# Optimization experiments

Measured on AMD Instinct MI355X. Metric: run time of the kernel, lower is better.

Reference implementation:

```python
import jax, jax.numpy as jnp
import numpy as np

N_NODES = 50000
N_EDGES = 800000


def _glorot(key, shape):
    fan_in, fan_out = shape
    lim = float(np.sqrt(6.0 / (fan_in + fan_out)))
    return jax.random.uniform(key, shape, jnp.float32, -lim, lim)


def setup_inputs() -> dict:
    key = jax.random.key(0)
    ks = jax.random.split(key, 8)
    x = jax.random.normal(ks[0], (N_NODES, 2), jnp.float32)
    edge_index = jax.random.randint(ks[1], (2, N_EDGES), 0, N_NODES, jnp.int64)
    edge_weight = jax.random.uniform(ks[2], (N_EDGES,), jnp.float32)
    return {
        "x": x,
        "edge_index": edge_index,
        "edge_weight": edge_weight,
        "W1": _glorot(ks[3], (2, 128)),
        "b1": jnp.zeros((128,), jnp.float32),
        "W2": _glorot(ks[4], (128, 64)),
        "b2": jnp.zeros((64,), jnp.float32),
        "W3": _glorot(ks[5], (64, 1)),
        "b3": jnp.zeros((1,), jnp.float32),
    }


def _gcn_conv(x, W, b, src, dst, ew, n_nodes):
    # PyG GCNConv with normalize=False: out[i] = sum_{e:(j->i)} ew[e] * (x_j @ W) + b
    h = x @ W                       # [N, F_out] tiny GEMM
    msg = h[src] * ew[:, None]      # [E, F_out] gather + scale
    out = jax.ops.segment_sum(msg, dst, num_segments=n_nodes)  # scatter-add
    return out + b


def reference(x, edge_index, edge_weight, W1, b1, W2, b2, W3, b3):
    src, dst = edge_index[0], edge_index[1]  # source_to_target flow: aggregate at dst
    n = x.shape[0]
    h1 = jax.nn.relu(_gcn_conv(x, W1, b1, src, dst, edge_weight, n))
    # dropout is a no-op in eval mode
    h2 = jax.nn.relu(_gcn_conv(h1, W2, b2, src, dst, edge_weight, n))
    h3 = _gcn_conv(h2, W3, b3, src, dst, edge_weight, n)  # [N, 1]
    return h3.squeeze(-1)  # [N]
```

## Files before the change

kernel.cpp:

```cpp
#include <hip/hip_runtime.h>
#include <hip/hip_fp16.h>

#define N_NODES 50000
#define N_EDGES 800000
#define BSHIFT 7
#define NBKT 391
#define CAP 3072
#define TILE 2048
#define BIN_THREADS 512
#define SL_THREADS 512

typedef _Float16 f16x8 __attribute__((ext_vector_type(8)));
typedef float f32x4 __attribute__((ext_vector_type(4)));
typedef float f32x2 __attribute__((ext_vector_type(2)));

__device__ __forceinline__ float edge_w(unsigned p) {
    return __half2float(__ushort_as_half((unsigned short)(p >> 16)));
}

__device__ __forceinline__ unsigned char f32_to_fp8(float v) {
    int w = __builtin_amdgcn_cvt_pk_fp8_f32(v, v, 0, false);
    return (unsigned char)(w & 0xFF);
}

__global__ __launch_bounds__(BIN_THREADS) void bin_edges(
    const int* __restrict__ src, const int* __restrict__ dstA,
    const float* __restrict__ ew, int* __restrict__ bcur,
    uint2* __restrict__ brec) {
    __shared__ unsigned pk[TILE];
    __shared__ unsigned short sdst[TILE];
    __shared__ uint2 rec[TILE];
    __shared__ int cnt[NBKT];
    __shared__ int lofs[NBKT];
    __shared__ int cbase[NBKT];
    __shared__ int scn[BIN_THREADS];

    int t = threadIdx.x;
    int e0 = blockIdx.x * TILE;
    int nmax = N_EDGES - e0;
    if (nmax > TILE) nmax = TILE;
    if (nmax < 0) nmax = 0;
    if (t < NBKT) cnt[t] = 0;
    __syncthreads();
    for (int i = t; i < nmax; i += BIN_THREADS) {
        int e = e0 + i;
        int d = dstA[e];
        unsigned hw = (unsigned)__half_as_ushort(__float2half(ew[e]));
        pk[i] = (unsigned)src[e] | (hw << 16);
        sdst[i] = (unsigned short)d;
        atomicAdd(&cnt[d >> BSHIFT], 1);
    }
    __syncthreads();
    int v = (t < NBKT) ? cnt[t] : 0;
    scn[t] = v;
    __syncthreads();
    for (int off = 1; off < BIN_THREADS; off <<= 1) {
        int u = (t >= off) ? scn[t - off] : 0;
        __syncthreads();
        scn[t] += u;
        __syncthreads();
    }
    if (t < NBKT) {
        lofs[t] = scn[t] - v;
        cbase[t] = t * CAP + (v ? atomicAdd(&bcur[t], v) : 0);
        cnt[t] = 0;
    }
    __syncthreads();
    for (int i = t; i < nmax; i += BIN_THREADS) {
        int d = sdst[i];
        int bk = d >> BSHIFT;
        int pos = lofs[bk] + atomicAdd(&cnt[bk], 1);
        rec[pos] = make_uint2(pk[i], (unsigned)d);
    }
    __syncthreads();
    for (int i = t; i < nmax; i += BIN_THREADS) {
        uint2 r = rec[i];
        int bk = (int)(r.y >> BSHIFT);
        int g = cbase[bk] + (i - lofs[bk]);
        brec[g] = r;
    }
}

__global__ __launch_bounds__(SL_THREADS) void sort_l1(
    const int* __restrict__ bcur, const uint2* __restrict__ brec,
    const float* __restrict__ x,
    const float* __restrict__ W1, const float* __restrict__ b1,
    const float* __restrict__ W2,
    unsigned* __restrict__ sorted, int2* __restrict__ rowspan,
    unsigned char* __restrict__ t2) {
    __shared__ unsigned spk[CAP];
    __shared__ unsigned short sdl[CAP];
    __shared__ int nh[128], scn[128], lcur[128];
    __shared__ float nodeA[128], nodeB[128];
    __shared__ __align__(16) __half w2t[64][136];
    __shared__ __align__(16) float w1r0[128];
    __shared__ __align__(16) float w1r1[128];
    __shared__ __align__(16) float b1s[128];

    int b = blockIdx.x;
    int t = threadIdx.x;
    int base = b * CAP;
    int n = bcur[b];
    if (n > CAP) n = CAP;

    for (int idx = t; idx < 128 * 64; idx += SL_THREADS) {
        int k = idx >> 6, nn = idx & 63;
        w2t[nn][k] = __float2half(W2[idx]);
    }
    if (t < 128) {
        w1r0[t] = W1[t];
        w1r1[t] = W1[128 + t];
        b1s[t]  = b1[t];
        nh[t] = 0;
        lcur[t] = 0;
        nodeA[t] = 0.f;
        nodeB[t] = 0.f;
    }
    __syncthreads();

    for (int e = t; e < n; e += SL_THREADS) {
        uint2 r = brec[base + e];
        spk[e] = r.x;
        int d = (int)(r.y & 127u);
        sdl[e] = (unsigned short)d;
        atomicAdd(&nh[d], 1);
    }
    __syncthreads();

    int vv = 0;
    if (t < 128) { vv = nh[t]; scn[t] = vv; }
    __syncthreads();
    for (int off = 1; off < 128; off <<= 1) {
        int u = (t < 128 && t >= off) ? scn[t - off] : 0;
        __syncthreads();
        if (t < 128) scn[t] += u;
        __syncthreads();
    }
    if (t < 128) {
        int ex = scn[t] - vv;
        int node = (b << BSHIFT) + t;
        if (node < N_NODES) rowspan[node] = make_int2(base + ex, base + ex + vv);
        nh[t] = ex;
    }
    __syncthreads();

    for (int e = t; e < n; e += SL_THREADS) {
        unsigned p = spk[e];
        int dlow = sdl[e];
        int pos = base + nh[dlow] + atomicAdd(&lcur[dlow], 1);
        sorted[pos] = p;
        float w = edge_w(p);
        float2 xv = ((const float2*)x)[p & 0xFFFF];
        atomicAdd(&nodeA[dlow], w * xv.x);
        atomicAdd(&nodeB[dlow], w * xv.y);
    }
    __syncthreads();

    int wave = t >> 6, lane = t & 63;
    int m0 = wave * 16;
    int fr = lane & 15;
    int kb = (lane >> 4) * 8;
    float a0 = nodeA[m0 + fr];
    float a1 = nodeB[m0 + fr];
    f32x4 acc0 = {0.f, 0.f, 0.f, 0.f};
    f32x4 acc1 = {0.f, 0.f, 0.f, 0.f};
    f32x4 acc2 = {0.f, 0.f, 0.f, 0.f};
    f32x4 acc3 = {0.f, 0.f, 0.f, 0.f};
#pragma unroll
    for (int k0 = 0; k0 < 128; k0 += 32) {
        f16x8 av;
#pragma unroll
        for (int j = 0; j < 8; j++) {
            int k = k0 + kb + j;
            float h = fmaxf(fmaf(a0, w1r0[k], fmaf(a1, w1r1[k], b1s[k])), 0.f);
            av[j] = (_Float16)h;
        }
        f16x8 bv0 = *(const f16x8*)&w2t[ 0 + fr][k0 + kb];
        f16x8 bv1 = *(const f16x8*)&w2t[16 + fr][k0 + kb];
        f16x8 bv2 = *(const f16x8*)&w2t[32 + fr][k0 + kb];
        f16x8 bv3 = *(const f16x8*)&w2t[48 + fr][k0 + kb];
        acc0 = __builtin_amdgcn_mfma_f32_16x16x32_f16(av, bv0, acc0, 0, 0, 0);
        acc1 = __builtin_amdgcn_mfma_f32_16x16x32_f16(av, bv1, acc1, 0, 0, 0);
        acc2 = __builtin_amdgcn_mfma_f32_16x16x32_f16(av, bv2, acc2, 0, 0, 0);
        acc3 = __builtin_amdgcn_mfma_f32_16x16x32_f16(av, bv3, acc3, 0, 0, 0);
    }
    int rowb = (b << BSHIFT) + m0 + (lane >> 4) * 4;
#pragma unroll
    for (int r = 0; r < 4; r++) {
        int node = rowb + r;
        if (node < N_NODES) {
            unsigned char* o = t2 + node * 64 + fr;
            o[0]  = f32_to_fp8(acc0[r]);
            o[16] = f32_to_fp8(acc1[r]);
            o[32] = f32_to_fp8(acc2[r]);
            o[48] = f32_to_fp8(acc3[r]);
        }
    }
}

__global__ void gather2_dot3(const int2* __restrict__ rowspan, const unsigned* __restrict__ sorted,
                             const unsigned char* __restrict__ t2, const float* __restrict__ b2,
                             const float* __restrict__ W3, float* __restrict__ t3) {
    int gtid = blockIdx.x * blockDim.x + threadIdx.x;
    int node = gtid >> 6;
    int lane = threadIdx.x & 63;
    if (node >= N_NODES) return;
    int eg  = lane >> 3;
    int fli = lane & 7;
    int2 sp = rowspan[node];
    float a0 = 0.f, a1 = 0.f, a2 = 0.f, a3 = 0.f, a4 = 0.f, a5 = 0.f, a6 = 0.f, a7 = 0.f;
    int e = sp.x + eg;
    for (; e + 8 < sp.y; e += 16) {
        unsigned p0 = sorted[e];
        unsigned p1 = sorted[e + 8];
        uint2 q0 = *(const uint2*)(t2 + (p0 & 0xFFFF) * 64 + fli * 8);
        uint2 q1 = *(const uint2*)(t2 + (p1 & 0xFFFF) * 64 + fli * 8);
        float w0 = edge_w(p0), w1 = edge_w(p1);
        f32x2 f;
        f = __builtin_amdgcn_cvt_pk_f32_fp8(q0.x, false); a0 = fmaf(w0, f.x, a0); a1 = fmaf(w0, f.y, a1);
        f = __builtin_amdgcn_cvt_pk_f32_fp8(q0.x, true);  a2 = fmaf(w0, f.x, a2); a3 = fmaf(w0, f.y, a3);
        f = __builtin_amdgcn_cvt_pk_f32_fp8(q0.y, false); a4 = fmaf(w0, f.x, a4); a5 = fmaf(w0, f.y, a5);
        f = __builtin_amdgcn_cvt_pk_f32_fp8(q0.y, true);  a6 = fmaf(w0, f.x, a6); a7 = fmaf(w0, f.y, a7);
        f = __builtin_amdgcn_cvt_pk_f32_fp8(q1.x, false); a0 = fmaf(w1, f.x, a0); a1 = fmaf(w1, f.y, a1);
        f = __builtin_amdgcn_cvt_pk_f32_fp8(q1.x, true);  a2 = fmaf(w1, f.x, a2); a3 = fmaf(w1, f.y, a3);
        f = __builtin_amdgcn_cvt_pk_f32_fp8(q1.y, false); a4 = fmaf(w1, f.x, a4); a5 = fmaf(w1, f.y, a5);
        f = __builtin_amdgcn_cvt_pk_f32_fp8(q1.y, true);  a6 = fmaf(w1, f.x, a6); a7 = fmaf(w1, f.y, a7);
    }
    if (e < sp.y) {
        unsigned p = sorted[e];
        uint2 q = *(const uint2*)(t2 + (p & 0xFFFF) * 64 + fli * 8);
        float w = edge_w(p);
        f32x2 f;
        f = __builtin_amdgcn_cvt_pk_f32_fp8(q.x, false); a0 = fmaf(w, f.x, a0); a1 = fmaf(w, f.y, a1);
        f = __builtin_amdgcn_cvt_pk_f32_fp8(q.x, true);  a2 = fmaf(w, f.x, a2); a3 = fmaf(w, f.y, a3);
        f = __builtin_amdgcn_cvt_pk_f32_fp8(q.y, false); a4 = fmaf(w, f.x, a4); a5 = fmaf(w, f.y, a5);
        f = __builtin_amdgcn_cvt_pk_f32_fp8(q.y, true);  a6 = fmaf(w, f.x, a6); a7 = fmaf(w, f.y, a7);
    }
#pragma unroll
    for (int off = 8; off < 64; off <<= 1) {
        a0 += __shfl_xor(a0, off); a1 += __shfl_xor(a1, off);
        a2 += __shfl_xor(a2, off); a3 += __shfl_xor(a3, off);
        a4 += __shfl_xor(a4, off); a5 += __shfl_xor(a5, off);
        a6 += __shfl_xor(a6, off); a7 += __shfl_xor(a7, off);
    }
    float4 bA = *(const float4*)(b2 + fli * 8);
    float4 bB = *(const float4*)(b2 + fli * 8 + 4);
    float4 wA = *(const float4*)(W3 + fli * 8);
    float4 wB = *(const float4*)(W3 + fli * 8 + 4);
    float h = fmaxf(a0 + bA.x, 0.f) * wA.x + fmaxf(a1 + bA.y, 0.f) * wA.y +
              fmaxf(a2 + bA.z, 0.f) * wA.z + fmaxf(a3 + bA.w, 0.f) * wA.w +
              fmaxf(a4 + bB.x, 0.f) * wB.x + fmaxf(a5 + bB.y, 0.f) * wB.y +
              fmaxf(a6 + bB.z, 0.f) * wB.z + fmaxf(a7 + bB.w, 0.f) * wB.w;
#pragma unroll
    for (int off = 1; off < 8; off <<= 1) h += __shfl_xor(h, off);
    if (lane == 0) t3[node] = h;
}

__global__ void gather3(const int2* __restrict__ rowspan, const unsigned* __restrict__ sorted,
                        const float* __restrict__ t3, const float* __restrict__ b3,
                        float* __restrict__ out) {
    int gtid = blockIdx.x * blockDim.x + threadIdx.x;
    int wid = gtid >> 6;
    int lane = threadIdx.x & 63;
    int sub = lane >> 4;
    int sl  = lane & 15;
    int node = wid * 4 + sub;
    if (node >= N_NODES) return;
    int2 sp = rowspan[node];
    float acc = 0.f;
    for (int e = sp.x + sl; e < sp.y; e += 16) {
        unsigned p = sorted[e];
        acc = fmaf(edge_w(p), t3[p & 0xFFFF], acc);
    }
#pragma unroll
    for (int off = 1; off < 16; off <<= 1) acc += __shfl_xor(acc, off);
    if (sl == 0) out[node] = acc + b3[0];
}

extern "C" void kernel_launch(void* const* d_in, const int* in_sizes, int n_in,
                              void* d_out, int out_size, void* d_ws, size_t ws_size,
                              hipStream_t stream) {
    const float* x  = (const float*)d_in[0];
    const int*   ei = (const int*)d_in[1];
    const float* ew = (const float*)d_in[2];
    const float* W1 = (const float*)d_in[3];
    const float* b1 = (const float*)d_in[4];
    const float* W2 = (const float*)d_in[5];
    const float* b2 = (const float*)d_in[6];
    const float* W3 = (const float*)d_in[7];
    const float* b3 = (const float*)d_in[8];
    float* out = (float*)d_out;

    const int* src = ei;
    const int* dst = ei + N_EDGES;

    char* p = (char*)d_ws;
    int*  bcur    = (int*)p;            p += NBKT * sizeof(int);
    p = (char*)(((uintptr_t)p + 15) & ~(uintptr_t)15);
    int2* rowspan = (int2*)p;           p += N_NODES * sizeof(int2);
    uint2* brec   = (uint2*)p;          p += (long)NBKT * CAP * sizeof(uint2);
    unsigned* sorted = (unsigned*)p;    p += (long)NBKT * CAP * sizeof(unsigned);
    unsigned char* t2 = (unsigned char*)p; p += 64L * N_NODES;
    float* t3     = (float*)p;          p += N_NODES * sizeof(float);

    hipMemsetAsync(bcur, 0, NBKT * sizeof(int), stream);

    bin_edges<<<NBKT, BIN_THREADS, 0, stream>>>(src, dst, ew, bcur, brec);

    sort_l1<<<NBKT, SL_THREADS, 0, stream>>>(bcur, brec, x, W1, b1, W2, sorted, rowspan, t2);

    gather2_dot3<<<(N_NODES * 64 + 255) / 256, 256, 0, stream>>>(rowspan, sorted, t2, b2, W3, t3);

    gather3<<<((N_NODES + 3) / 4 * 64 + 255) / 256, 256, 0, stream>>>(rowspan, sorted, t3, b3, out);
}
```

Before: 139.5 us.

## Use wave-shuffle scans, register-held edges, and narrower gather3 node groups

Replaces the barrier-heavy shared-memory prefix scans in bin_edges and sort_l1 with wavefront shuffle scans plus a small cross-wave combine. In sort_l1 the records are kept in registers (up to 6 per thread), layer-1 aggregation moves into the first pass, and edges are scattered into LDS and then written to global memory contiguously instead of through scattered global writes. gather3 now assigns 8 lanes per node instead of 16, so each wave covers 8 nodes. The fixed 6-per-thread register array relies on CAP/SL_THREADS = 6, and the LDS atomic ordering still makes the within-node edge order nondeterministic.

```diff
diff --git a/kernel.cpp b/kernel.cpp
--- a/kernel.cpp
+++ b/kernel.cpp
@@ -33,9 +33,11 @@
     __shared__ int cnt[NBKT];
     __shared__ int lofs[NBKT];
     __shared__ int cbase[NBKT];
-    __shared__ int scn[BIN_THREADS];
+    __shared__ int wsum[8];
+    __shared__ int wpre[8];
 
     int t = threadIdx.x;
+    int lane = t & 63, wid = t >> 6;
     int e0 = blockIdx.x * TILE;
     int nmax = N_EDGES - e0;
     if (nmax > TILE) nmax = TILE;
@@ -52,16 +54,23 @@
     }
     __syncthreads();
     int v = (t < NBKT) ? cnt[t] : 0;
-    scn[t] = v;
-    __syncthreads();
-    for (int off = 1; off < BIN_THREADS; off <<= 1) {
-        int u = (t >= off) ? scn[t - off] : 0;
-        __syncthreads();
-        scn[t] += u;
-        __syncthreads();
-    }
+    int s = v;
+#pragma unroll
+    for (int off = 1; off < 64; off <<= 1) {
+        int u = __shfl_up(s, off);
+        if (lane >= off) s += u;
+    }
+    if (lane == 63) wsum[wid] = s;
+    __syncthreads();
+    if (t < 8) {
+        int a = 0;
+        for (int i = 0; i < t; i++) a += wsum[i];
+        wpre[t] = a;
+    }
+    __syncthreads();
+    int incl = s + wpre[wid];
     if (t < NBKT) {
-        lofs[t] = scn[t] - v;
+        lofs[t] = incl - v;
         cbase[t] = t * CAP + (v ? atomicAdd(&bcur[t], v) : 0);
         cnt[t] = 0;
     }
@@ -89,16 +98,17 @@
     unsigned* __restrict__ sorted, int2* __restrict__ rowspan,
     unsigned char* __restrict__ t2) {
     __shared__ unsigned spk[CAP];
-    __shared__ unsigned short sdl[CAP];
-    __shared__ int nh[128], scn[128], lcur[128];
+    __shared__ int nh[128], lcur[128];
     __shared__ float nodeA[128], nodeB[128];
     __shared__ __align__(16) __half w2t[64][136];
     __shared__ __align__(16) float w1r0[128];
     __shared__ __align__(16) float w1r1[128];
     __shared__ __align__(16) float b1s[128];
+    __shared__ int wsum2[2];
 
     int b = blockIdx.x;
     int t = threadIdx.x;
+    int lane = t & 63, wid = t >> 6;
     int base = b * CAP;
     int n = bcur[b];
     if (n > CAP) n = CAP;
@@ -118,45 +128,54 @@
     }
     __syncthreads();
 
-    for (int e = t; e < n; e += SL_THREADS) {
-        uint2 r = brec[base + e];
-        spk[e] = r.x;
-        int d = (int)(r.y & 127u);
-        sdl[e] = (unsigned short)d;
-        atomicAdd(&nh[d], 1);
-    }
-    __syncthreads();
-
-    int vv = 0;
-    if (t < 128) { vv = nh[t]; scn[t] = vv; }
-    __syncthreads();
-    for (int off = 1; off < 128; off <<= 1) {
-        int u = (t < 128 && t >= off) ? scn[t - off] : 0;
-        __syncthreads();
-        if (t < 128) scn[t] += u;
-        __syncthreads();
-    }
+    unsigned rp[6];
+    int rd[6];
+#pragma unroll
+    for (int i = 0; i < 6; i++) {
+        int e = t + i * SL_THREADS;
+        if (e < n) {
+            uint2 r = brec[base + e];
+            rp[i] = r.x;
+            rd[i] = (int)(r.y & 127u);
+            atomicAdd(&nh[rd[i]], 1);
+            float w = edge_w(r.x);
+            float2 xv = ((const float2*)x)[r.x & 0xFFFF];
+            atomicAdd(&nodeA[rd[i]], w * xv.x);
+            atomicAdd(&nodeB[rd[i]], w * xv.y);
+        }
+    }
+    __syncthreads();
+
+    int v = (t < 128) ? nh[t] : 0;
+    int s = v;
+#pragma unroll
+    for (int off = 1; off < 64; off <<= 1) {
+        int u = __shfl_up(s, off);
+        if (lane >= off) s += u;
+    }
+    if (lane == 63 && wid < 2) wsum2[wid] = s;
+    __syncthreads();
     if (t < 128) {
-        int ex = scn[t] - vv;
+        int incl = s + (wid ? wsum2[0] : 0);
+        int ex = incl - v;
         int node = (b << BSHIFT) + t;
-        if (node < N_NODES) rowspan[node] = make_int2(base + ex, base + ex + vv);
+        if (node < N_NODES) rowspan[node] = make_int2(base + ex, base + ex + v);
         nh[t] = ex;
     }
     __syncthreads();
 
-    for (int e = t; e < n; e += SL_THREADS) {
-        unsigned p = spk[e];
-        int dlow = sdl[e];
-        int pos = base + nh[dlow] + atomicAdd(&lcur[dlow], 1);
-        sorted[pos] = p;
-        float w = edge_w(p);
-        float2 xv = ((const float2*)x)[p & 0xFFFF];
-        atomicAdd(&nodeA[dlow], w * xv.x);
-        atomicAdd(&nodeB[dlow], w * xv.y);
-    }
-    __syncthreads();
-
-    int wave = t >> 6, lane = t & 63;
+#pragma unroll
+    for (int i = 0; i < 6; i++) {
+        int e = t + i * SL_THREADS;
+        if (e < n) {
+            int pos = nh[rd[i]] + atomicAdd(&lcur[rd[i]], 1);
+            spk[pos] = rp[i];
+        }
+    }
+    __syncthreads();
+    for (int e = t; e < n; e += SL_THREADS) sorted[base + e] = spk[e];
+
+    int wave = t >> 6;
     int m0 = wave * 16;
     int fr = lane & 15;
     int kb = (lane >> 4) * 8;
@@ -184,7 +203,7 @@
         acc2 = __builtin_amdgcn_mfma_f32_16x16x32_f16(av, bv2, acc2, 0, 0, 0);
         acc3 = __builtin_amdgcn_mfma_f32_16x16x32_f16(av, bv3, acc3, 0, 0, 0);
     }
-    int rowb = (b << BSHIFT) + m0 + (lane >> 4) * 4;
+    int rowb = (b << BSHIFT) + m0 + ((lane >> 4) & 3) * 4;
 #pragma unroll
     for (int r = 0; r < 4; r++) {
         int node = rowb + r;
@@ -262,18 +281,18 @@
     int gtid = blockIdx.x * blockDim.x + threadIdx.x;
     int wid = gtid >> 6;
     int lane = threadIdx.x & 63;
-    int sub = lane >> 4;
-    int sl  = lane & 15;
-    int node = wid * 4 + sub;
+    int sub = lane >> 3;
+    int sl  = lane & 7;
+    int node = wid * 8 + sub;
     if (node >= N_NODES) return;
     int2 sp = rowspan[node];
     float acc = 0.f;
-    for (int e = sp.x + sl; e < sp.y; e += 16) {
+    for (int e = sp.x + sl; e < sp.y; e += 8) {
         unsigned p = sorted[e];
         acc = fmaf(edge_w(p), t3[p & 0xFFFF], acc);
     }
 #pragma unroll
-    for (int off = 1; off < 16; off <<= 1) acc += __shfl_xor(acc, off);
+    for (int off = 1; off < 8; off <<= 1) acc += __shfl_xor(acc, off);
     if (sl == 0) out[node] = acc + b3[0];
 }
 
@@ -311,5 +330,5 @@
 
     gather2_dot3<<<(N_NODES * 64 + 255) / 256, 256, 0, stream>>>(rowspan, sorted, t2, b2, W3, t3);
 
-    gather3<<<((N_NODES + 3) / 4 * 64 + 255) / 256, 256, 0, stream>>>(rowspan, sorted, t3, b3, out);
-}
+    gather3<<<((N_NODES + 7) / 8 * 64 + 255) / 256, 256, 0, stream>>>(rowspan, sorted, t3, b3, out);
+}
```

Measured after the change: 136.8 us, median of 2. Within noise of the previous version (-1.9%).
